# Performance work log

Measured on AMD Instinct MI355X. Metric: run time of the kernel, lower is better.

The kernel has to match this reference:

```python
import jax, jax.numpy as jnp
import numpy as np


def setup_inputs() -> dict:
    key = jax.random.key(0)
    ks = jax.random.split(key, 12)
    B, C, H, W = 8, 256, 64, 64
    inter = C // 8
    s = 0.05  # weight scale keeps q.k logits in a stable softmax range
    f32 = jnp.float32
    x = jax.random.normal(ks[0], (B, C, H, W), f32)
    Wq = jax.random.normal(ks[1], (inter, C), f32) * s
    bq = jnp.zeros((inter,), f32)
    Wk = jax.random.normal(ks[2], (inter, C), f32) * s
    bk = jnp.zeros((inter,), f32)
    Wv = jax.random.normal(ks[3], (C, C), f32) * s
    bv = jnp.zeros((C,), f32)
    gamma = jnp.full((1,), 0.5, f32)  # learnable residual scale (init 0 in torch; 0.5 exercises the path)
    Wg1 = jax.random.normal(ks[4], (inter, C), f32) * s
    bg1 = jnp.zeros((inter,), f32)
    Wg2 = jax.random.normal(ks[5], (C, inter), f32) * s
    bg2 = jnp.zeros((C,), f32)
    return {"x": x, "Wq": Wq, "bq": bq, "Wk": Wk, "bk": bk, "Wv": Wv, "bv": bv,
            "gamma": gamma, "Wg1": Wg1, "bg1": bg1, "Wg2": Wg2, "bg2": bg2}


def reference(x, Wq, bq, Wk, bk, Wv, bv, gamma, Wg1, bg1, Wg2, bg2):
    B, C, H, W = x.shape
    N = H * W
    xf = x.reshape(B, C, N)  # [B,C,N]
    # 1x1 convs == per-pixel linear projections
    q = jnp.einsum('oc,bcn->bon', Wq, xf) + bq[None, :, None]  # [B,inter,N]
    k = jnp.einsum('oc,bcn->bon', Wk, xf) + bk[None, :, None]  # [B,inter,N]
    v = jnp.einsum('oc,bcn->bon', Wv, xf) + bv[None, :, None]  # [B,C,N]
    # attention[b,n,m] = softmax_m( q[b,:,n] . k[b,:,m] )
    attn = jax.nn.softmax(jnp.einsum('bin,bim->bnm', q, k), axis=-1)  # [B,N,N]
    # out[b,c,n] = sum_m v[b,c,m] * attn[b,n,m]
    out = jnp.einsum('bcm,bnm->bcn', v, attn)  # [B,C,N]
    out = gamma[0] * out + xf
    # gated global pooling branch: GAP -> 1x1 conv -> ReLU -> 1x1 conv -> Sigmoid
    gp = xf.mean(axis=-1)  # [B,C]
    h = jax.nn.relu(jnp.einsum('oc,bc->bo', Wg1, gp) + bg1)  # [B,inter]
    ga = jax.nn.sigmoid(jnp.einsum('co,bo->bc', Wg2, h) + bg2)  # [B,C]
    out = out * ga[:, :, None] + out
    return out.reshape(B, C, H, W)
```

## Files before the change

kernel.cpp:

```cpp
#include <hip/hip_runtime.h>

typedef unsigned short u16;
typedef unsigned int   u32;
typedef short s16x4 __attribute__((ext_vector_type(4)));
typedef u16 u16x4 __attribute__((ext_vector_type(4)));
typedef u16 u16x8 __attribute__((ext_vector_type(8)));
typedef __bf16 bf16x8 __attribute__((ext_vector_type(8)));
typedef float f32x4 __attribute__((ext_vector_type(4)));
typedef float f32x2 __attribute__((ext_vector_type(2)));
typedef u32 u32x2v __attribute__((ext_vector_type(2)));
typedef u32 u32x4v __attribute__((ext_vector_type(4)));

#define NB 8
#define NC 256
#define NI 32
#define NN 4096
#define LOG2E 1.4426950408889634f
#define POFF 64.0f

__device__ __forceinline__ float bf2f(u16 v) {
    u32 u = ((u32)v) << 16;
    return __builtin_bit_cast(float, u);
}
__device__ __forceinline__ u32 cvtpk_bf16(float lo, float hi) {
    u32 r;
    asm("v_cvt_pk_bf16_f32 %0, %1, %2" : "=v"(r) : "v"(lo), "v"(hi));
    return r;
}
__device__ __forceinline__ u16 f2bf_hw(float f) {
    u32 r;
    asm("v_cvt_pk_bf16_f32 %0, %1, %1" : "=v"(r) : "v"(f));
    return (u16)r;
}
__device__ __forceinline__ void permswap32(u32& a, u32& b) {
#if __has_builtin(__builtin_amdgcn_permlane32_swap)
    auto r = __builtin_amdgcn_permlane32_swap(a, b, false, false);
    a = (u32)r[0]; b = (u32)r[1];
#else
    int ln = (int)(threadIdx.x & 63);
    u32 a2 = (u32)__shfl_xor((int)a, 32, 64);
    u32 b2 = (u32)__shfl_xor((int)b, 32, 64);
    u32 na = (ln < 32) ? a : b2;
    u32 nb = (ln < 32) ? a2 : b;
    a = na; b = nb;
#endif
}
__device__ __forceinline__ void permswap16(u32& a, u32& b) {
#if __has_builtin(__builtin_amdgcn_permlane16_swap)
    auto r = __builtin_amdgcn_permlane16_swap(a, b, false, false);
    a = (u32)r[0]; b = (u32)r[1];
#else
    int q = (int)((threadIdx.x >> 4) & 1);
    u32 az = (u32)__shfl_xor((int)a, 16, 64);
    u32 bz = (u32)__shfl_xor((int)b, 16, 64);
    u32 na = q ? bz : a;
    u32 nb = q ? b  : az;
    a = na; b = nb;
#endif
}
__device__ __forceinline__ bool is_f32_mode(const void* graw) {
    return ((const u16*)graw)[0] == 0;
}
__device__ __forceinline__ float ldb(bool f32m, const void* p, int idx) {
    return f32m ? ((const float*)p)[idx] : bf2f(((const u16*)p)[idx]);
}
__device__ __forceinline__ bf16x8 ldwf(const float* p) {
    f32x4 a = *(const f32x4*)p;
    f32x4 c = *(const f32x4*)(p + 4);
    u32x4v r;
    r.x = cvtpk_bf16(a[0], a[1]); r.y = cvtpk_bf16(a[2], a[3]);
    r.z = cvtpk_bf16(c[0], c[1]); r.w = cvtpk_bf16(c[2], c[3]);
    return __builtin_bit_cast(bf16x8, r);
}

__global__ __launch_bounds__(256) void proj_kernel(
    const void* xr, const void* graw,
    const void* Wq, const void* bq, const void* Wk, const void* bk,
    const void* Wv, const void* bv,
    u16* __restrict__ qt, u16* __restrict__ kt, u16* __restrict__ v,
    float* __restrict__ gp)
{
    bool f32m = is_f32_mode(graw);
    int t = threadIdx.x;

    if (blockIdx.x >= 512) {
        int row = blockIdx.x - 512;
        int base = row * 4096 + t * 16;
        float s = 0.f;
        if (f32m) {
            const float* xs = (const float*)xr;
#pragma unroll
            for (int k = 0; k < 4; ++k) {
                f32x4 a = *(const f32x4*)(xs + base + k * 4);
                s += (a[0] + a[1]) + (a[2] + a[3]);
            }
        } else {
            const u16* xs = (const u16*)xr;
#pragma unroll
            for (int k = 0; k < 2; ++k) {
                u16x8 a = *(const u16x8*)(xs + base + k * 8);
#pragma unroll
                for (int j = 0; j < 8; ++j) s += bf2f(a[j]);
            }
        }
#pragma unroll
        for (int off = 1; off <= 32; off <<= 1) s += __shfl_xor(s, off, 64);
        __shared__ float ws[4];
        if ((t & 63) == 0) ws[t >> 6] = s;
        __syncthreads();
        if (t == 0) gp[row] = (ws[0] + ws[1] + ws[2] + ws[3]) * (1.0f / NN);
        return;
    }

    __shared__ __attribute__((aligned(16))) u16 xs[64][264];

    int lane = t & 63;
    int wave = t >> 6;
    int b    = blockIdx.x >> 6;
    int m0   = (blockIdx.x & 63) << 6;
    int l15  = lane & 15;
    int quad = lane >> 4;

    {
        int c0 = wave * 64;
        if (f32m) {
            const float* xb = (const float*)xr + (size_t)b * NC * NN + m0 + lane;
#pragma unroll
            for (int ci = 0; ci < 64; ci += 4) {
                int c = c0 + ci;
                float a0 = xb[(size_t)(c    ) * NN];
                float a1 = xb[(size_t)(c + 1) * NN];
                float a2 = xb[(size_t)(c + 2) * NN];
                float a3 = xb[(size_t)(c + 3) * NN];
                u32x2v p2;
                p2.x = cvtpk_bf16(a0, a1);
                p2.y = cvtpk_bf16(a2, a3);
                *(u32x2v*)&xs[lane][c] = p2;
            }
        } else {
            const u16* xb = (const u16*)xr + (size_t)b * NC * NN + m0 + lane;
#pragma unroll
            for (int ci = 0; ci < 64; ci += 4) {
                int c = c0 + ci;
                u16x4 p4;
                p4[0] = xb[(size_t)(c    ) * NN];
                p4[1] = xb[(size_t)(c + 1) * NN];
                p4[2] = xb[(size_t)(c + 2) * NN];
                p4[3] = xb[(size_t)(c + 3) * NN];
                *(u16x4*)&xs[lane][c] = p4;
            }
        }
    }
    __syncthreads();

    const f32x4 zero4 = {};
    f32x4 acc[5][4];
#pragma unroll
    for (int i = 0; i < 5; ++i)
#pragma unroll
        for (int mt = 0; mt < 4; ++mt) acc[i][mt] = zero4;

    int obase = wave * 80;

    const u16*   wsrc16[5];
    const float* wsrc32[5];
#pragma unroll
    for (int i = 0; i < 5; ++i) {
        int R0 = obase + i * 16;
        if (f32m) {
            const float* s = (R0 < 32) ? (const float*)Wq + (size_t)R0 * 256
                           : (R0 < 64) ? (const float*)Wk + (size_t)(R0 - 32) * 256
                                       : (const float*)Wv + (size_t)(R0 - 64) * 256;
            wsrc32[i] = s + l15 * 256 + quad * 8;
            wsrc16[i] = nullptr;
        } else {
            const u16* s = (R0 < 32) ? (const u16*)Wq + (size_t)R0 * 256
                         : (R0 < 64) ? (const u16*)Wk + (size_t)(R0 - 32) * 256
                                     : (const u16*)Wv + (size_t)(R0 - 64) * 256;
            wsrc16[i] = s + l15 * 256 + quad * 8;
            wsrc32[i] = nullptr;
        }
    }

    bf16x8 af[5];
#pragma unroll
    for (int i = 0; i < 5; ++i)
        af[i] = f32m ? ldwf(wsrc32[i]) : *(const bf16x8*)(wsrc16[i]);

#pragma unroll
    for (int kc = 0; kc < 8; ++kc) {
        bf16x8 afn[5], bfr[4];
        if (kc < 7) {
#pragma unroll
            for (int i = 0; i < 5; ++i)
                afn[i] = f32m ? ldwf(wsrc32[i] + (kc + 1) * 32)
                              : *(const bf16x8*)(wsrc16[i] + (kc + 1) * 32);
        }
#pragma unroll
        for (int mt = 0; mt < 4; ++mt)
            bfr[mt] = *(const bf16x8*)&xs[mt * 16 + l15][kc * 32 + quad * 8];
#pragma unroll
        for (int i = 0; i < 5; ++i)
#pragma unroll
            for (int mt = 0; mt < 4; ++mt)
                acc[i][mt] = __builtin_amdgcn_mfma_f32_16x16x32_bf16(af[i], bfr[mt], acc[i][mt], 0, 0, 0);
        if (kc < 7) {
#pragma unroll
            for (int i = 0; i < 5; ++i) af[i] = afn[i];
        }
    }

    __syncthreads();

    if (wave == 0) {
#pragma unroll
        for (int i = 0; i < 4; ++i) {
#pragma unroll
            for (int mt = 0; mt < 4; ++mt) {
                float tv[4];
#pragma unroll
                for (int r = 0; r < 4; ++r) {
                    int o = i * 16 + quad * 4 + r;
                    if (o < 32) tv[r] = LOG2E * (acc[i][mt][r] + ldb(f32m, bq, o));
                    else        tv[r] = acc[i][mt][r] + ldb(f32m, bk, o - 32);
                }
                u32x2v p2;
                p2.x = cvtpk_bf16(tv[0], tv[1]);
                p2.y = cvtpk_bf16(tv[2], tv[3]);
                *(u32x2v*)&xs[mt * 16 + l15][i * 16 + quad * 4] = p2;
            }
        }
        int m = m0 + lane;
        u16* qrow = qt + (size_t)(b * NN + m) * NI;
        u16* krow = kt + (size_t)(b * NN + m) * NI;
#pragma unroll
        for (int j = 0; j < 4; ++j) *(u16x8*)(qrow + j * 8) = *(const u16x8*)&xs[lane][j * 8];
#pragma unroll
        for (int j = 0; j < 4; ++j) *(u16x8*)(krow + j * 8) = *(const u16x8*)&xs[lane][32 + j * 8];
#pragma unroll
        for (int mt = 0; mt < 4; ++mt) {
#pragma unroll
            for (int r = 0; r < 4; ++r) {
                int c = quad * 4 + r;
                v[(size_t)(b * NC + c) * NN + m0 + mt * 16 + l15] = f2bf_hw(acc[4][mt][r] + ldb(f32m, bv, c));
            }
        }
    } else {
#pragma unroll
        for (int i = 0; i < 5; ++i) {
#pragma unroll
            for (int mt = 0; mt < 4; ++mt) {
#pragma unroll
                for (int r = 0; r < 4; ++r) {
                    int c = wave * 80 + i * 16 + quad * 4 + r - 64;
                    v[(size_t)(b * NC + c) * NN + m0 + mt * 16 + l15] = f2bf_hw(acc[i][mt][r] + ldb(f32m, bv, c));
                }
            }
        }
    }
}

__global__ __launch_bounds__(256) void gate_kernel(
    const float* __restrict__ gp, const void* graw,
    const void* Wg1, const void* bg1, const void* Wg2, const void* bg2,
    float* __restrict__ gmul)
{
    bool f32m = is_f32_mode(graw);
    int b = blockIdx.x;
    int t = threadIdx.x;
    __shared__ float gps[NC];
    __shared__ float hs[NI];
    gps[t] = gp[b * NC + t];
    __syncthreads();
    if (t < NI) {
        float a = ldb(f32m, bg1, t);
        for (int c = 0; c < NC; ++c) a += ldb(f32m, Wg1, t * NC + c) * gps[c];
        hs[t] = a > 0.f ? a : 0.f;
    }
    __syncthreads();
    float a = ldb(f32m, bg2, t);
#pragma unroll
    for (int i = 0; i < NI; ++i) a += ldb(f32m, Wg2, t * NI + i) * hs[i];
    float sig = 1.f / (1.f + __expf(-a));
    gmul[b * NC + t] = 1.f + sig;
}

__global__ __launch_bounds__(512, 4) void flash_kernel(
    const u16* __restrict__ qt, const u16* __restrict__ kt, const u16* __restrict__ v,
    const void* xr, const void* graw,
    const float* __restrict__ gmul, void* outp)
{
    __shared__ __attribute__((aligned(16))) u16 vs[2][2][NC][40];

    bool f32m = is_f32_mode(graw);

    int t    = threadIdx.x;
    int lane = t & 63;
    int wave = t >> 6;
    int b    = blockIdx.x & 7;
    int nblk = (blockIdx.x >> 3) << 6;
    int n0   = nblk + (wave >> 1) * 16;
    int c0   = (wave & 1) * 128;
    int l15  = lane & 15;
    int quad = lane >> 4;

    const f32x4 mneg = {-POFF, -POFF, -POFF, -POFF};

    bf16x8 qf = *(const bf16x8*)(qt + (size_t)(b * NN + n0 + l15) * NI + quad * 8);

    f32x4 acc[8];
#pragma unroll
    for (int ct = 0; ct < 8; ++ct) acc[ct] = f32x4{};
    f32x2 psum2 = {};

    int sc = t >> 2;
    int sm = (t & 3) * 8;
    const u16* vb0 = v + (size_t)(b * NC + sc) * NN + sm;
    const u16* vb1 = v + (size_t)(b * NC + sc + 128) * NN + sm;
    const u16* ktb = kt + (size_t)(b * NN + l15) * NI + quad * 8;

    u16x8 sr0, sr1, sr2, sr3;
    sr0 = *(const u16x8*)(vb0);        sr1 = *(const u16x8*)(vb1);
    sr2 = *(const u16x8*)(vb0 + 32);   sr3 = *(const u16x8*)(vb1 + 32);
    *(u16x8*)&vs[0][0][sc][sm]       = sr0;
    *(u16x8*)&vs[0][0][sc + 128][sm] = sr1;
    *(u16x8*)&vs[0][1][sc][sm]       = sr2;
    *(u16x8*)&vs[0][1][sc + 128][sm] = sr3;
    sr0 = *(const u16x8*)(vb0 + 64);   sr1 = *(const u16x8*)(vb1 + 64);
    sr2 = *(const u16x8*)(vb0 + 96);   sr3 = *(const u16x8*)(vb1 + 96);
    bf16x8 ktA[2], ktB[2];
    ktA[0] = *(const bf16x8*)(ktb);
    ktA[1] = *(const bf16x8*)(ktb + (size_t)16 * NI);
    ktB[0] = *(const bf16x8*)(ktb + (size_t)32 * NI);
    ktB[1] = *(const bf16x8*)(ktb + (size_t)48 * NI);
    __syncthreads();

    for (int it = 0; it < 64; ++it) {
        int p = it & 1;
        bool wmore = (it < 63);
        bool lmore = (it < 62);

        if (wmore) {
            *(u16x8*)&vs[p ^ 1][0][sc][sm]       = sr0;
            *(u16x8*)&vs[p ^ 1][0][sc + 128][sm] = sr1;
            *(u16x8*)&vs[p ^ 1][1][sc][sm]       = sr2;
            *(u16x8*)&vs[p ^ 1][1][sc + 128][sm] = sr3;
        }
        if (lmore) {
            int cb = it * 64 + 128;
            sr0 = *(const u16x8*)(vb0 + cb);
            sr1 = *(const u16x8*)(vb1 + cb);
            sr2 = *(const u16x8*)(vb0 + cb + 32);
            sr3 = *(const u16x8*)(vb1 + cb + 32);
        }

#pragma unroll
        for (int h = 0; h < 2; ++h) {
            bf16x8* ktX = (h == 0) ? ktA : ktB;

            f32x4 sf[2];
#pragma unroll
            for (int mt = 0; mt < 2; ++mt)
                sf[mt] = __builtin_amdgcn_mfma_f32_16x16x32_bf16(ktX[mt], qf, mneg, 0, 0, 0);

            bf16x8 va8[8];
#pragma unroll
            for (int ct = 0; ct < 8; ++ct)
                va8[ct] = *(const bf16x8*)&vs[p][h][c0 + ct * 16 + l15][quad * 8];

            if (wmore) {
                int mg = it * 64 + 64 + h * 32;
                ktX[0] = *(const bf16x8*)(ktb + (size_t)mg * NI);
                ktX[1] = *(const bf16x8*)(ktb + (size_t)(mg + 16) * NI);
            }

            float pp[2][4];
#pragma unroll
            for (int mt = 0; mt < 2; ++mt)
#pragma unroll
                for (int r = 0; r < 4; ++r)
                    pp[mt][r] = __builtin_amdgcn_exp2f(sf[mt][r]);
            f32x2 t0; t0.x = pp[0][0]; t0.y = pp[0][1];
            f32x2 t1; t1.x = pp[0][2]; t1.y = pp[0][3];
            f32x2 t2; t2.x = pp[1][0]; t2.y = pp[1][1];
            f32x2 t3; t3.x = pp[1][2]; t3.y = pp[1][3];
            psum2 += (t0 + t1) + (t2 + t3);
            u32 A0 = cvtpk_bf16(pp[0][0], pp[0][1]);
            u32 A1 = cvtpk_bf16(pp[0][2], pp[0][3]);
            u32 B0 = cvtpk_bf16(pp[1][0], pp[1][1]);
            u32 B1 = cvtpk_bf16(pp[1][2], pp[1][3]);
            permswap32(A0, B0); permswap16(A0, B0);
            permswap32(A1, B1); permswap16(A1, B1);
            u32x4v f; f.x = A0; f.y = A1; f.z = B0; f.w = B1;
            bf16x8 pfr8 = __builtin_bit_cast(bf16x8, f);

#pragma unroll
            for (int ct = 0; ct < 8; ++ct)
                acc[ct] = __builtin_amdgcn_mfma_f32_16x16x32_bf16(va8[ct], pfr8, acc[ct], 0, 0, 0);
        }

        __syncthreads();
    }

    float s = psum2.x + psum2.y;
    s += __shfl_xor(s, 16, 64);
    s += __shfl_xor(s, 32, 64);
    float inv = 1.f / s;
    float gam = f32m ? ((const float*)graw)[0] : bf2f(((const u16*)graw)[0]);
    int n = n0 + l15;

#pragma unroll
    for (int ct = 0; ct < 8; ++ct) {
        int cb = c0 + ct * 16 + quad * 4;
        f32x4 gm4 = *(const f32x4*)&gmul[b * NC + cb];
#pragma unroll
        for (int r = 0; r < 4; ++r) {
            size_t off = (size_t)(b * NC + cb + r) * NN + n;
            float xv = f32m ? ((const float*)xr)[off] : bf2f(((const u16*)xr)[off]);
            float val = (gam * acc[ct][r] * inv + xv) * gm4[r];
            if (f32m) ((float*)outp)[off] = val;
            else      ((u16*)outp)[off]  = f2bf_hw(val);
        }
    }
}

extern "C" void kernel_launch(void* const* d_in, const int* in_sizes, int n_in,
                              void* d_out, int out_size, void* d_ws, size_t ws_size,
                              hipStream_t stream)
{
    const void* x     = d_in[0];
    const void* Wq    = d_in[1];
    const void* bq    = d_in[2];
    const void* Wk    = d_in[3];
    const void* bk    = d_in[4];
    const void* Wv    = d_in[5];
    const void* bvp   = d_in[6];
    const void* gamma = d_in[7];
    const void* Wg1   = d_in[8];
    const void* bg1   = d_in[9];
    const void* Wg2   = d_in[10];
    const void* bg2   = d_in[11];

    char* ws = (char*)d_ws;
    u16*   qt   = (u16*)  (ws + 33951744);
    u16*   kt   = (u16*)  (ws + 36048896);
    u16*   v    = (u16*)  (ws + 38146048);
    float* gp   = (float*)(ws + 54923264);
    float* gmul = (float*)(ws + 54931456);

    proj_kernel<<<2560, 256, 0, stream>>>(x, gamma, Wq, bq, Wk, bk, Wv, bvp,
                                          qt, kt, v, gp);
    gate_kernel<<<NB, 256, 0, stream>>>(gp, gamma, Wg1, bg1, Wg2, bg2, gmul);
    flash_kernel<<<NB * 64, 512, 0, stream>>>(qt, kt, v, x, gamma, gmul, d_out);
}
```

Baseline: 277.4 us.

## Retile flash waves to 32 rows x 64 channels and split GAP kernel

Each wave in the flash kernel now covers 32 query rows and 64 channels instead of 16 rows and 128 channels. Every V fragment read from LDS is reused across two query tiles, which halves LDS reads per MFMA, but each wave now computes twice the QK scores and exponentials. The change also staggers which half-tile each wave processes first, raises wave priority around MFMA bursts, and moves global average pooling out of the projection kernel into its own kernel. That separate kernel adds one launch.

```diff
diff --git a/kernel.cpp b/kernel.cpp
--- a/kernel.cpp
+++ b/kernel.cpp
@@ -73,47 +73,48 @@
     return __builtin_bit_cast(bf16x8, r);
 }
 
+__global__ __launch_bounds__(256) void gap_kernel(
+    const void* xr, const void* graw, float* __restrict__ gp)
+{
+    bool f32m = is_f32_mode(graw);
+    int row = blockIdx.x, t = threadIdx.x;
+    int base = row * 4096 + t * 16;
+    float s = 0.f;
+    if (f32m) {
+        const float* xs = (const float*)xr;
+#pragma unroll
+        for (int k = 0; k < 4; ++k) {
+            f32x4 a = *(const f32x4*)(xs + base + k * 4);
+            s += (a[0] + a[1]) + (a[2] + a[3]);
+        }
+    } else {
+        const u16* xs = (const u16*)xr;
+#pragma unroll
+        for (int k = 0; k < 2; ++k) {
+            u16x8 a = *(const u16x8*)(xs + base + k * 8);
+#pragma unroll
+            for (int j = 0; j < 8; ++j) s += bf2f(a[j]);
+        }
+    }
+#pragma unroll
+    for (int off = 1; off <= 32; off <<= 1) s += __shfl_xor(s, off, 64);
+    __shared__ float ws[4];
+    if ((t & 63) == 0) ws[t >> 6] = s;
+    __syncthreads();
+    if (t == 0) gp[row] = (ws[0] + ws[1] + ws[2] + ws[3]) * (1.0f / NN);
+}
+
 __global__ __launch_bounds__(256) void proj_kernel(
     const void* xr, const void* graw,
     const void* Wq, const void* bq, const void* Wk, const void* bk,
     const void* Wv, const void* bv,
-    u16* __restrict__ qt, u16* __restrict__ kt, u16* __restrict__ v,
-    float* __restrict__ gp)
+    u16* __restrict__ qt, u16* __restrict__ kt, u16* __restrict__ v)
 {
+    __shared__ __attribute__((aligned(16))) u16 xs[64][264];
+
     bool f32m = is_f32_mode(graw);
-    int t = threadIdx.x;
-
-    if (blockIdx.x >= 512) {
-        int row = blockIdx.x - 512;
-        int base = row * 4096 + t * 16;
-        float s = 0.f;
-        if (f32m) {
-            const float* xs = (const float*)xr;
-#pragma unroll
-            for (int k = 0; k < 4; ++k) {
-                f32x4 a = *(const f32x4*)(xs + base + k * 4);
-                s += (a[0] + a[1]) + (a[2] + a[3]);
-            }
-        } else {
-            const u16* xs = (const u16*)xr;
-#pragma unroll
-            for (int k = 0; k < 2; ++k) {
-                u16x8 a = *(const u16x8*)(xs + base + k * 8);
-#pragma unroll
-                for (int j = 0; j < 8; ++j) s += bf2f(a[j]);
-            }
-        }
-#pragma unroll
-        for (int off = 1; off <= 32; off <<= 1) s += __shfl_xor(s, off, 64);
-        __shared__ float ws[4];
-        if ((t & 63) == 0) ws[t >> 6] = s;
-        __syncthreads();
-        if (t == 0) gp[row] = (ws[0] + ws[1] + ws[2] + ws[3]) * (1.0f / NN);
-        return;
-    }
-
-    __shared__ __attribute__((aligned(16))) u16 xs[64][264];
-
+
+    int t    = threadIdx.x;
     int lane = t & 63;
     int wave = t >> 6;
     int b    = blockIdx.x >> 6;
@@ -299,19 +300,25 @@
     int wave = t >> 6;
     int b    = blockIdx.x & 7;
     int nblk = (blockIdx.x >> 3) << 6;
-    int n0   = nblk + (wave >> 1) * 16;
-    int c0   = (wave & 1) * 128;
+    int n0   = nblk + (wave >> 2) * 32;
+    int c0   = (wave & 3) * 64;
     int l15  = lane & 15;
     int quad = lane >> 4;
+    int hord = wave & 1;
 
     const f32x4 mneg = {-POFF, -POFF, -POFF, -POFF};
 
-    bf16x8 qf = *(const bf16x8*)(qt + (size_t)(b * NN + n0 + l15) * NI + quad * 8);
-
-    f32x4 acc[8];
-#pragma unroll
-    for (int ct = 0; ct < 8; ++ct) acc[ct] = f32x4{};
-    f32x2 psum2 = {};
+    bf16x8 qf[2];
+#pragma unroll
+    for (int n16 = 0; n16 < 2; ++n16)
+        qf[n16] = *(const bf16x8*)(qt + (size_t)(b * NN + n0 + n16 * 16 + l15) * NI + quad * 8);
+
+    f32x4 acc[2][4];
+#pragma unroll
+    for (int n16 = 0; n16 < 2; ++n16)
+#pragma unroll
+        for (int ct = 0; ct < 4; ++ct) acc[n16][ct] = f32x4{};
+    float psum[2] = {0.f, 0.f};
 
     int sc = t >> 2;
     int sm = (t & 3) * 8;
@@ -355,17 +362,22 @@
         }
 
 #pragma unroll
-        for (int h = 0; h < 2; ++h) {
+        for (int hh = 0; hh < 2; ++hh) {
+            int h = hh ^ hord;
             bf16x8* ktX = (h == 0) ? ktA : ktB;
 
-            f32x4 sf[2];
+            __builtin_amdgcn_s_setprio(1);
+            f32x4 sf[2][2];
 #pragma unroll
             for (int mt = 0; mt < 2; ++mt)
-                sf[mt] = __builtin_amdgcn_mfma_f32_16x16x32_bf16(ktX[mt], qf, mneg, 0, 0, 0);
-
-            bf16x8 va8[8];
-#pragma unroll
-            for (int ct = 0; ct < 8; ++ct)
+#pragma unroll
+                for (int n16 = 0; n16 < 2; ++n16)
+                    sf[n16][mt] = __builtin_amdgcn_mfma_f32_16x16x32_bf16(ktX[mt], qf[n16], mneg, 0, 0, 0);
+            __builtin_amdgcn_s_setprio(0);
+
+            bf16x8 va8[4];
+#pragma unroll
+            for (int ct = 0; ct < 4; ++ct)
                 va8[ct] = *(const bf16x8*)&vs[p][h][c0 + ct * 16 + l15][quad * 8];
 
             if (wmore) {
@@ -374,52 +386,64 @@
                 ktX[1] = *(const bf16x8*)(ktb + (size_t)(mg + 16) * NI);
             }
 
-            float pp[2][4];
-#pragma unroll
-            for (int mt = 0; mt < 2; ++mt)
-#pragma unroll
-                for (int r = 0; r < 4; ++r)
-                    pp[mt][r] = __builtin_amdgcn_exp2f(sf[mt][r]);
-            f32x2 t0; t0.x = pp[0][0]; t0.y = pp[0][1];
-            f32x2 t1; t1.x = pp[0][2]; t1.y = pp[0][3];
-            f32x2 t2; t2.x = pp[1][0]; t2.y = pp[1][1];
-            f32x2 t3; t3.x = pp[1][2]; t3.y = pp[1][3];
-            psum2 += (t0 + t1) + (t2 + t3);
-            u32 A0 = cvtpk_bf16(pp[0][0], pp[0][1]);
-            u32 A1 = cvtpk_bf16(pp[0][2], pp[0][3]);
-            u32 B0 = cvtpk_bf16(pp[1][0], pp[1][1]);
-            u32 B1 = cvtpk_bf16(pp[1][2], pp[1][3]);
-            permswap32(A0, B0); permswap16(A0, B0);
-            permswap32(A1, B1); permswap16(A1, B1);
-            u32x4v f; f.x = A0; f.y = A1; f.z = B0; f.w = B1;
-            bf16x8 pfr8 = __builtin_bit_cast(bf16x8, f);
-
-#pragma unroll
-            for (int ct = 0; ct < 8; ++ct)
-                acc[ct] = __builtin_amdgcn_mfma_f32_16x16x32_bf16(va8[ct], pfr8, acc[ct], 0, 0, 0);
+            bf16x8 pfr8[2];
+#pragma unroll
+            for (int n16 = 0; n16 < 2; ++n16) {
+                float pp[2][4];
+#pragma unroll
+                for (int mt = 0; mt < 2; ++mt)
+#pragma unroll
+                    for (int r = 0; r < 4; ++r)
+                        pp[mt][r] = __builtin_amdgcn_exp2f(sf[n16][mt][r]);
+                psum[n16] += ((pp[0][0] + pp[0][1]) + (pp[0][2] + pp[0][3]))
+                           + ((pp[1][0] + pp[1][1]) + (pp[1][2] + pp[1][3]));
+                u32 A0 = cvtpk_bf16(pp[0][0], pp[0][1]);
+                u32 A1 = cvtpk_bf16(pp[0][2], pp[0][3]);
+                u32 B0 = cvtpk_bf16(pp[1][0], pp[1][1]);
+                u32 B1 = cvtpk_bf16(pp[1][2], pp[1][3]);
+                permswap32(A0, B0); permswap16(A0, B0);
+                permswap32(A1, B1); permswap16(A1, B1);
+                u32x4v f; f.x = A0; f.y = A1; f.z = B0; f.w = B1;
+                pfr8[n16] = __builtin_bit_cast(bf16x8, f);
+            }
+
+            __builtin_amdgcn_s_setprio(1);
+#pragma unroll
+            for (int ct = 0; ct < 4; ++ct)
+#pragma unroll
+                for (int n16 = 0; n16 < 2; ++n16)
+                    acc[n16][ct] = __builtin_amdgcn_mfma_f32_16x16x32_bf16(va8[ct], pfr8[n16], acc[n16][ct], 0, 0, 0);
+            __builtin_amdgcn_s_setprio(0);
         }
 
         __syncthreads();
     }
 
-    float s = psum2.x + psum2.y;
-    s += __shfl_xor(s, 16, 64);
-    s += __shfl_xor(s, 32, 64);
-    float inv = 1.f / s;
+    float inv[2];
+#pragma unroll
+    for (int n16 = 0; n16 < 2; ++n16) {
+        float s = psum[n16];
+        s += __shfl_xor(s, 16, 64);
+        s += __shfl_xor(s, 32, 64);
+        inv[n16] = 1.f / s;
+    }
     float gam = f32m ? ((const float*)graw)[0] : bf2f(((const u16*)graw)[0]);
-    int n = n0 + l15;
-
-#pragma unroll
-    for (int ct = 0; ct < 8; ++ct) {
-        int cb = c0 + ct * 16 + quad * 4;
-        f32x4 gm4 = *(const f32x4*)&gmul[b * NC + cb];
-#pragma unroll
-        for (int r = 0; r < 4; ++r) {
-            size_t off = (size_t)(b * NC + cb + r) * NN + n;
-            float xv = f32m ? ((const float*)xr)[off] : bf2f(((const u16*)xr)[off]);
-            float val = (gam * acc[ct][r] * inv + xv) * gm4[r];
-            if (f32m) ((float*)outp)[off] = val;
-            else      ((u16*)outp)[off]  = f2bf_hw(val);
+
+#pragma unroll
+    for (int n16 = 0; n16 < 2; ++n16) {
+        int n = n0 + n16 * 16 + l15;
+#pragma unroll
+        for (int ct = 0; ct < 4; ++ct) {
+            int cb = c0 + ct * 16 + quad * 4;
+            f32x4 gm4 = *(const f32x4*)&gmul[b * NC + cb];
+#pragma unroll
+            for (int r = 0; r < 4; ++r) {
+                size_t off = (size_t)(b * NC + cb + r) * NN + n;
+                float xv = f32m ? ((const float*)xr)[off] : bf2f(((const u16*)xr)[off]);
+                float val = (gam * acc[n16][ct][r] * inv[n16] + xv) * gm4[r];
+                if (f32m) ((float*)outp)[off] = val;
+                else      ((u16*)outp)[off]  = f2bf_hw(val);
+            }
         }
     }
 }
@@ -448,8 +472,9 @@
     float* gp   = (float*)(ws + 54923264);
     float* gmul = (float*)(ws + 54931456);
 
-    proj_kernel<<<2560, 256, 0, stream>>>(x, gamma, Wq, bq, Wk, bk, Wv, bvp,
-                                          qt, kt, v, gp);
+    gap_kernel<<<2048, 256, 0, stream>>>(x, gamma, gp);
+    proj_kernel<<<512, 256, 0, stream>>>(x, gamma, Wq, bq, Wk, bk, Wv, bvp,
+                                         qt, kt, v);
     gate_kernel<<<NB, 256, 0, stream>>>(gp, gamma, Wg1, bg1, Wg2, bg2, gmul);
     flash_kernel<<<NB * 64, 512, 0, stream>>>(qt, kt, v, x, gamma, gmul, d_out);
 }
```

Result: slower. 549.1 us (+98.0%).
